# Kernel tuning notes

Hardware: AMD Instinct MI355X
Metric: run time of the kernel (lower is better)

The kernel has to match this reference:

```python
import jax, jax.numpy as jnp
import numpy as np

B, L, C = 32, 8192, 32
P, S = 16, 8
N = (L - P) // S + 1  # 1023 tokens
K = 16
HID = max(16, 2 * K)  # 32
STD_FLOOR = 0.01


def setup_inputs() -> dict:
    key = jax.random.key(0)
    ks = jax.random.split(key, 8)
    return {
        "x": jax.random.normal(ks[0], (B, L, C), jnp.float32),
        "freq_features": jax.random.normal(ks[1], (B * C, N, K), jnp.float32),
        "alpha_w1": jax.random.normal(ks[2], (K, HID), jnp.float32) * 0.1,
        "alpha_b1": jnp.zeros((HID,), jnp.float32),
        "alpha_w2": jax.random.normal(ks[3], (HID, 1), jnp.float32) * 0.1,
        "alpha_b2": jnp.zeros((1,), jnp.float32),
        "beta_w1": jax.random.normal(ks[4], (K, HID), jnp.float32) * 0.1,
        "beta_b1": jnp.zeros((HID,), jnp.float32),
        "beta_w2": jax.random.normal(ks[5], (HID, 1), jnp.float32) * 0.1,
        "beta_b2": jnp.zeros((1,), jnp.float32),
        "affine_scale": jnp.ones((C,), jnp.float32),
        "affine_bias": jnp.zeros((C,), jnp.float32),
        "n_tokens": N,
    }


def _gate_mlp(ff, w1, b1, w2, b2):
    # Linear -> exact GELU (torch default) -> Linear -> sigmoid, squeeze last dim
    h = jax.nn.gelu(ff @ w1 + b1, approximate=False)
    return jax.nn.sigmoid((h @ w2 + b2)[..., 0])


def reference(x, freq_features, alpha_w1, alpha_b1, alpha_w2, alpha_b2,
              beta_w1, beta_b1, beta_w2, beta_b2, affine_scale, affine_bias,
              n_tokens):
    Bx, Lx, Cx = x.shape
    Nn = n_tokens
    # global stats over time dim (biased var)
    mu_g = jnp.mean(x, axis=1, keepdims=True)                     # [B,1,C]
    var_g = jnp.mean((x - mu_g) ** 2, axis=1, keepdims=True)
    std_g = jnp.sqrt(jnp.maximum(var_g, STD_FLOOR * STD_FLOOR))
    # local per-patch stats via strided gather (equivalent to unfold)
    idx = jnp.arange(Nn)[:, None] * S + jnp.arange(P)[None, :]    # [N,P]
    patches = x[:, idx, :]                                        # [B,N,P,C]
    mu_l = jnp.mean(patches, axis=2)                              # [B,N,C]
    var_l = jnp.mean((patches - mu_l[:, :, None, :]) ** 2, axis=2)
    std_l = jnp.sqrt(jnp.maximum(var_l, STD_FLOOR * STD_FLOOR))   # [B,N,C]
    # map each timestep to nearest patch center
    centers = jnp.arange(Nn, dtype=jnp.float32) * S + P / 2.0
    dist = jnp.abs(jnp.arange(Lx, dtype=jnp.float32)[:, None] - centers[None, :])
    tok_per_time = jnp.argmin(dist, axis=1)                       # [L] int
    mu_l_t = mu_l[:, tok_per_time, :]                             # [B,L,C]
    std_l_t = std_l[:, tok_per_time, :]
    # freq-conditioned mixing gate alpha per token, gathered per timestep
    ff = freq_features.reshape(Bx, Cx, Nn, -1)                    # [B,C,N,K]
    alpha_tok = _gate_mlp(ff, alpha_w1, alpha_b1, alpha_w2, alpha_b2)  # [B,C,N]
    beta_tok = _gate_mlp(ff, beta_w1, beta_b1, beta_w2, beta_b2)       # [B,C,N] (ctx only)
    alpha_t = jnp.transpose(alpha_tok[:, :, tok_per_time], (0, 2, 1))  # [B,L,C]
    # normalize and mix
    x_norm_local = jnp.clip((x - mu_l_t) / jnp.maximum(std_l_t, STD_FLOOR), -30.0, 30.0)
    x_norm_global = jnp.clip((x - mu_g) / jnp.maximum(std_g, STD_FLOOR), -30.0, 30.0)
    x_norm = alpha_t * x_norm_local + (1.0 - alpha_t) * x_norm_global
    x_norm = x_norm * affine_scale[None, None, :] + affine_bias[None, None, :]
    return x_norm
```

## Files before the change

kernel.cpp:

```cpp
#include <hip/hip_runtime.h>
#include <math.h>

#define BB   32
#define LL   8192
#define CC   32
#define NTOK 1023
#define KK   16
#define HID  32

typedef short  bf16x8 __attribute__((ext_vector_type(8)));
typedef float  f32x4v __attribute__((ext_vector_type(4)));
typedef unsigned int u32;
typedef unsigned short ushort_t;

__device__ __forceinline__ float4 f4add(float4 a, float4 b) {
    return make_float4(a.x + b.x, a.y + b.y, a.z + b.z, a.w + b.w);
}
__device__ __forceinline__ float4 f4fma(float4 a, float4 b, float4 c) {
    return make_float4(fmaf(a.x, b.x, c.x), fmaf(a.y, b.y, c.y),
                       fmaf(a.z, b.z, c.z), fmaf(a.w, b.w, c.w));
}
__device__ __forceinline__ float4 shflx4(float4 v, int m) {
    return make_float4(__shfl_xor(v.x, m, 64), __shfl_xor(v.y, m, 64),
                       __shfl_xor(v.z, m, 64), __shfl_xor(v.w, m, 64));
}
__device__ __forceinline__ float ex2(float x) {
    return __builtin_amdgcn_exp2f(x);
}
__device__ __forceinline__ u32 pkbf16(float a, float b) {
    u32 r;
    asm("v_cvt_pk_bf16_f32 %0, %1, %2" : "=v"(r) : "v"(a), "v"(b));
    return r;
}

__global__ void __launch_bounds__(256)
kA_fused(const float* __restrict__ x,  const float* __restrict__ ff,
         const float* __restrict__ w1g, const float* __restrict__ b1,
         const float* __restrict__ w2,  const float* __restrict__ b2,
         float* __restrict__ ps, float* __restrict__ pq,
         float* __restrict__ mu_l, float* __restrict__ rstd_l,
         float* __restrict__ alpha_a) {
    __shared__ float4 smem4[592];
    int t   = threadIdx.x;
    int idx = blockIdx.x;
    int r3  = idx % 3, q3 = idx / 3;

    if (r3 == 0) {
        float4* part_s = smem4;
        float4* part_q = part_s + 256;
        float4* halo_s = part_q + 256;
        float4* halo_q = halo_s + 8;
        float4* wred_s = halo_q + 8;
        float4* wred_q = wred_s + 32;

        int b  = q3 >> 5;
        int s  = q3 & 31;
        int c4 = t & 7, rgrp = t >> 3;
        const float4* xb = (const float4*)x + ((size_t)b * LL + s * 256) * 8;

        float4 v[8];
#pragma unroll
        for (int k = 0; k < 8; ++k)
            v[k] = xb[(rgrp * 8 + k) * 8 + c4];
        float4 s4 = make_float4(0.f, 0.f, 0.f, 0.f);
        float4 q4 = make_float4(0.f, 0.f, 0.f, 0.f);
#pragma unroll
        for (int k = 0; k < 8; ++k) {
            s4 = f4add(s4, v[k]);
            q4 = f4fma(v[k], v[k], q4);
        }
        part_s[t] = s4;
        part_q[t] = q4;

        if (t < 64) {
            float4 hs = make_float4(0.f, 0.f, 0.f, 0.f);
            float4 hq = make_float4(0.f, 0.f, 0.f, 0.f);
            if (s < 31) {
                float4 hv = xb[(256 + (t >> 3)) * 8 + c4];
                hs = hv; hq = f4fma(hv, hv, hq);
            }
            hs = f4add(hs, shflx4(hs, 8));  hq = f4add(hq, shflx4(hq, 8));
            hs = f4add(hs, shflx4(hs, 16)); hq = f4add(hq, shflx4(hq, 16));
            hs = f4add(hs, shflx4(hs, 32)); hq = f4add(hq, shflx4(hq, 32));
            if (t < 8) { halo_s[t] = hs; halo_q[t] = hq; }
        }

        float4 gs = s4, gq = q4;
        gs = f4add(gs, shflx4(gs, 8));  gq = f4add(gq, shflx4(gq, 8));
        gs = f4add(gs, shflx4(gs, 16)); gq = f4add(gq, shflx4(gq, 16));
        gs = f4add(gs, shflx4(gs, 32)); gq = f4add(gq, shflx4(gq, 32));
        if ((t & 56) == 0) {
            wred_s[(t >> 6) * 8 + c4] = gs;
            wred_q[(t >> 6) * 8 + c4] = gq;
        }
        __syncthreads();

        int nl = t >> 3;
        int n  = s * 32 + nl;
        if (n < NTOK) {
            float4 a  = (nl < 31) ? part_s[(nl + 1) * 8 + c4] : halo_s[c4];
            float4 bq = (nl < 31) ? part_q[(nl + 1) * 8 + c4] : halo_q[c4];
            float4 ts = f4add(part_s[t], a);
            float4 tq = f4add(part_q[t], bq);
            float4 mu = make_float4(ts.x * 0.0625f, ts.y * 0.0625f,
                                    ts.z * 0.0625f, ts.w * 0.0625f);
            float4 var;
            var.x = fmaxf(fmaf(-mu.x, mu.x, tq.x * 0.0625f), 1e-4f);
            var.y = fmaxf(fmaf(-mu.y, mu.y, tq.y * 0.0625f), 1e-4f);
            var.z = fmaxf(fmaf(-mu.z, mu.z, tq.z * 0.0625f), 1e-4f);
            var.w = fmaxf(fmaf(-mu.w, mu.w, tq.w * 0.0625f), 1e-4f);
            float4 rs = make_float4(1.f / sqrtf(var.x), 1.f / sqrtf(var.y),
                                    1.f / sqrtf(var.z), 1.f / sqrtf(var.w));
            size_t o = (size_t)(b * NTOK + n) * 8 + c4;
            ((float4*)mu_l)[o]   = mu;
            ((float4*)rstd_l)[o] = rs;
        }

        if (t < 8) {
            float4 a = f4add(f4add(wred_s[t], wred_s[8 + t]),
                             f4add(wred_s[16 + t], wred_s[24 + t]));
            float4 c = f4add(f4add(wred_q[t], wred_q[8 + t]),
                             f4add(wred_q[16 + t], wred_q[24 + t]));
            ((float4*)ps)[q3 * 8 + t] = a;
            ((float4*)pq)[q3 * 8 + t] = c;
        }
    } else {
        int a_id = q3 * 2 + (r3 - 1);
        int l  = t & 63, wv = t >> 6;
        bool active = (l < 32);

        int kb = 8 * ((l >> 4) & 1);
        int j0 = l & 15;
        union { u32 w[4]; bf16x8 v; } UA0, UA1;
#pragma unroll
        for (int p = 0; p < 4; ++p) {
            float a0 = w1g[(kb + 2*p)     * HID + j0];
            float a1 = w1g[(kb + 2*p + 1) * HID + j0];
            float a2 = w1g[(kb + 2*p)     * HID + j0 + 16];
            float a3 = w1g[(kb + 2*p + 1) * HID + j0 + 16];
            u32 u0 = pkbf16(a0, a1), u1 = pkbf16(a2, a3);
            UA0.w[p] = active ? u0 : 0u;
            UA1.w[p] = active ? u1 : 0u;
        }
        bf16x8 Alo = UA0.v, Ahi = UA1.v;

        int jg = 4 * (l >> 4);
        f32x4v b1lo = *(const f32x4v*)(b1 + jg);
        f32x4v b1hi = *(const f32x4v*)(b1 + 16 + jg);
        f32x4v w2lo = *(const f32x4v*)(w2 + jg);
        f32x4v w2hi = *(const f32x4v*)(w2 + 16 + jg);
        float b2s = b2[0];

        const float C0 = -2.302211325f;
        const float C1 = -0.102943702f;

        size_t rowbase = ((size_t)a_id * 4 + wv) * 128;
        const float4* fpc = (const float4*)ff + rowbase * 4
                          + (size_t)(l & 15) * 4 + ((l >> 4) & 1) * 2;

        float4 a0 = fpc[0],  a1 = fpc[1];
        float4 p0 = fpc[64], p1 = fpc[65];

        for (int it = 0; it < 8; ++it) {
            float4 f0 = a0, f1 = a1;
            a0 = p0; a1 = p1;
            if (it < 6) { p0 = fpc[128]; p1 = fpc[129]; }
            fpc += 64;

            union { u32 w[4]; bf16x8 v; } B;
            u32 w0 = pkbf16(f0.x, f0.y), w1v = pkbf16(f0.z, f0.w);
            u32 w2v = pkbf16(f1.x, f1.y), w3 = pkbf16(f1.z, f1.w);
            B.w[0] = active ? w0 : 0u;  B.w[1] = active ? w1v : 0u;
            B.w[2] = active ? w2v : 0u; B.w[3] = active ? w3 : 0u;

            f32x4v d0 = __builtin_amdgcn_mfma_f32_16x16x32_bf16(Alo, B.v, b1lo, 0, 0, 0);
            f32x4v d1 = __builtin_amdgcn_mfma_f32_16x16x32_bf16(Ahi, B.v, b1hi, 0, 0, 0);

            float partial = 0.f;
#pragma unroll
            for (int r = 0; r < 4; ++r) {
                float h  = d0[r];
                float a  = fmaf(h * h, C1, C0);
                float g  = h * __builtin_amdgcn_rcpf(1.0f + ex2(a * h));
                partial  = fmaf(g, w2lo[r], partial);
                float h2 = d1[r];
                float a2 = fmaf(h2 * h2, C1, C0);
                float g2 = h2 * __builtin_amdgcn_rcpf(1.0f + ex2(a2 * h2));
                partial  = fmaf(g2, w2hi[r], partial);
            }
            partial += __shfl_xor(partial, 16, 64);
            partial += __shfl_xor(partial, 32, 64);
            float outv = b2s + partial;
            float av = __builtin_amdgcn_rcpf(1.0f + ex2(-1.44269504f * outv));
            if (l < 16) alpha_a[rowbase + l] = av;
            rowbase += 16;
        }
    }
}

__global__ void k3b_transpose(const float* __restrict__ a_bcn,
                              float* __restrict__ a_bnc) {
    __shared__ float tile[32][33];
    int b  = blockIdx.x >> 5;
    int n0 = (blockIdx.x & 31) * 32;
    int tn = threadIdx.x & 31;
    int tc = threadIdx.x >> 5;
#pragma unroll
    for (int i = 0; i < 4; ++i) {
        int c = tc + 8 * i;
        int n = n0 + tn;
        float v = 0.f;
        if (n < NTOK) v = a_bcn[((size_t)(b * CC + c)) * NTOK + n];
        tile[c][tn] = v;
    }
    __syncthreads();
#pragma unroll
    for (int i = 0; i < 4; ++i) {
        int n = n0 + tc + 8 * i;
        if (n < NTOK) a_bnc[((size_t)(b * NTOK + n)) * CC + tn] = tile[tn][tc + 8 * i];
    }
}

__global__ void __launch_bounds__(256)
k4_main(const float4* __restrict__ x4,
        const float* __restrict__ ps, const float* __restrict__ pq,
        const float4* __restrict__ mul4, const float4* __restrict__ rsl4,
        const float4* __restrict__ al4,
        const float4* __restrict__ sc4, const float4* __restrict__ bi4,
        float4* __restrict__ out4) {
    __shared__ float red_s[8][32], red_q[8][32];
    __shared__ float mugs[32], rsgs[32];
    int t  = threadIdx.x;
    int i4 = blockIdx.x * 256 + t;
    int b  = i4 >> 16;

    {
        int c = t & 31, grp = t >> 5;
        float s = 0.f, q = 0.f;
#pragma unroll
        for (int i = 0; i < 4; ++i) {
            int sl = grp * 4 + i;
            s += ps[(b * 32 + sl) * 32 + c];
            q += pq[(b * 32 + sl) * 32 + c];
        }
        red_s[grp][c] = s; red_q[grp][c] = q;
        __syncthreads();
        if (t < 32) {
            float ss = 0.f, qq = 0.f;
#pragma unroll
            for (int g = 0; g < 8; ++g) { ss += red_s[g][t]; qq += red_q[g][t]; }
            float mu  = ss * (1.0f / LL);
            float var = fmaxf(qq * (1.0f / LL) - mu * mu, 1e-4f);
            mugs[t] = mu;
            rsgs[t] = 1.0f / sqrtf(var);
        }
        __syncthreads();
    }

    int c4 = i4 & 7;
    int l  = (i4 >> 3) & (LL - 1);
    int n  = (l >= 5) ? min((l - 5) >> 3, NTOK - 1) : 0;

    float4 xv = x4[i4];
    float4 mg = *(const float4*)(mugs + 4 * c4);
    float4 rg = *(const float4*)(rsgs + 4 * c4);
    int o4 = (b * NTOK + n) * 8 + c4;
    float4 ml = mul4[o4], rl = rsl4[o4], av = al4[o4];
    float4 s  = sc4[c4],  bi = bi4[c4];

    float4 y;
    {
        float xg = fminf(fmaxf((xv.x - mg.x) * rg.x, -30.f), 30.f);
        float xl = fminf(fmaxf((xv.x - ml.x) * rl.x, -30.f), 30.f);
        y.x = fmaf(av.x, xl - xg, xg) * s.x + bi.x;
    }
    {
        float xg = fminf(fmaxf((xv.y - mg.y) * rg.y, -30.f), 30.f);
        float xl = fminf(fmaxf((xv.y - ml.y) * rl.y, -30.f), 30.f);
        y.y = fmaf(av.y, xl - xg, xg) * s.y + bi.y;
    }
    {
        float xg = fminf(fmaxf((xv.z - mg.z) * rg.z, -30.f), 30.f);
        float xl = fminf(fmaxf((xv.z - ml.z) * rl.z, -30.f), 30.f);
        y.z = fmaf(av.z, xl - xg, xg) * s.z + bi.z;
    }
    {
        float xg = fminf(fmaxf((xv.w - mg.w) * rg.w, -30.f), 30.f);
        float xl = fminf(fmaxf((xv.w - ml.w) * rl.w, -30.f), 30.f);
        y.w = fmaf(av.w, xl - xg, xg) * s.w + bi.w;
    }
    out4[i4] = y;
}

extern "C" void kernel_launch(void* const* d_in, const int* in_sizes, int n_in,
                              void* d_out, int out_size, void* d_ws, size_t ws_size,
                              hipStream_t stream) {
    const float* x    = (const float*)d_in[0];
    const float* ff   = (const float*)d_in[1];
    const float* aw1  = (const float*)d_in[2];
    const float* ab1  = (const float*)d_in[3];
    const float* aw2  = (const float*)d_in[4];
    const float* ab2  = (const float*)d_in[5];
    const float* scal = (const float*)d_in[10];
    const float* bias = (const float*)d_in[11];
    float* out = (float*)d_out;

    float* wsf     = (float*)d_ws;
    float* ps      = wsf;
    float* pq      = wsf + 32768;
    float* mu_l    = wsf + 65536;
    float* rstd_l  = mu_l    + 1047552;
    float* alpha_a = rstd_l  + 1047552;
    float* alpha_t = alpha_a + 1047552;

    kA_fused<<<3070, 256, 0, stream>>>(x, ff, aw1, ab1, aw2, ab2,
                                       ps, pq, mu_l, rstd_l, alpha_a);
    k3b_transpose<<<BB * 32, 256, 0, stream>>>(alpha_a, alpha_t);
    k4_main<<<8192, 256, 0, stream>>>((const float4*)x, ps, pq,
                                      (const float4*)mu_l, (const float4*)rstd_l,
                                      (const float4*)alpha_t,
                                      (const float4*)scal, (const float4*)bias,
                                      (float4*)out);
}
```

Before: 47.61 us.

## Fuse alpha gate transpose into MLP kernel via shared-memory tile

The separate transpose kernel that converted the alpha gate from [B,C,N] to [B,N,C] is removed. Each MLP workgroup now handles 16 tokens across all 32 channels of one batch, keeps the 32x16 results in shared memory and writes them out already transposed. This removes one launch and a full write-then-read round trip of the alpha buffer. In exchange the freq-feature loads become strided by channel, token indices at the tail are clamped, and the grid grows slightly to 3072 blocks.

```diff
diff --git a/kernel.cpp b/kernel.cpp
--- a/kernel.cpp
+++ b/kernel.cpp
@@ -39,7 +39,7 @@
          const float* __restrict__ w2,  const float* __restrict__ b2,
          float* __restrict__ ps, float* __restrict__ pq,
          float* __restrict__ mu_l, float* __restrict__ rstd_l,
-         float* __restrict__ alpha_a) {
+         float* __restrict__ alpha_t) {
     __shared__ float4 smem4[592];
     int t   = threadIdx.x;
     int idx = blockIdx.x;
@@ -125,7 +125,10 @@
             ((float4*)pq)[q3 * 8 + t] = c;
         }
     } else {
+        float* als = (float*)smem4;
         int a_id = q3 * 2 + (r3 - 1);
+        int b    = a_id >> 6;
+        int n0   = (a_id & 63) * 16;
         int l  = t & 63, wv = t >> 6;
         bool active = (l < 32);
 
@@ -154,18 +157,20 @@
         const float C0 = -2.302211325f;
         const float C1 = -0.102943702f;
 
-        size_t rowbase = ((size_t)a_id * 4 + wv) * 128;
-        const float4* fpc = (const float4*)ff + rowbase * 4
-                          + (size_t)(l & 15) * 4 + ((l >> 4) & 1) * 2;
-
-        float4 a0 = fpc[0],  a1 = fpc[1];
-        float4 p0 = fpc[64], p1 = fpc[65];
+        int nlane = min(n0 + (l & 15), NTOK - 1);
+        size_t cbase = (size_t)(b * 32 + 8 * wv) * NTOK;
+        const float4* fpc = (const float4*)ff + (cbase + nlane) * 4
+                          + ((l >> 4) & 1) * 2;
+        const int STRD = NTOK * 4;
+
+        float4 a0 = fpc[0],     a1 = fpc[1];
+        float4 p0 = fpc[STRD],  p1 = fpc[STRD + 1];
 
         for (int it = 0; it < 8; ++it) {
             float4 f0 = a0, f1 = a1;
             a0 = p0; a1 = p1;
-            if (it < 6) { p0 = fpc[128]; p1 = fpc[129]; }
-            fpc += 64;
+            if (it < 6) { p0 = fpc[2 * STRD]; p1 = fpc[2 * STRD + 1]; }
+            fpc += STRD;
 
             union { u32 w[4]; bf16x8 v; } B;
             u32 w0 = pkbf16(f0.x, f0.y), w1v = pkbf16(f0.z, f0.w);
@@ -192,32 +197,18 @@
             partial += __shfl_xor(partial, 32, 64);
             float outv = b2s + partial;
             float av = __builtin_amdgcn_rcpf(1.0f + ex2(-1.44269504f * outv));
-            if (l < 16) alpha_a[rowbase + l] = av;
-            rowbase += 16;
-        }
-    }
-}
-
-__global__ void k3b_transpose(const float* __restrict__ a_bcn,
-                              float* __restrict__ a_bnc) {
-    __shared__ float tile[32][33];
-    int b  = blockIdx.x >> 5;
-    int n0 = (blockIdx.x & 31) * 32;
-    int tn = threadIdx.x & 31;
-    int tc = threadIdx.x >> 5;
-#pragma unroll
-    for (int i = 0; i < 4; ++i) {
-        int c = tc + 8 * i;
-        int n = n0 + tn;
-        float v = 0.f;
-        if (n < NTOK) v = a_bcn[((size_t)(b * CC + c)) * NTOK + n];
-        tile[c][tn] = v;
-    }
-    __syncthreads();
-#pragma unroll
-    for (int i = 0; i < 4; ++i) {
-        int n = n0 + tc + 8 * i;
-        if (n < NTOK) a_bnc[((size_t)(b * NTOK + n)) * CC + tn] = tile[tn][tc + 8 * i];
+            if (l < 16) als[(8 * wv + it) * 17 + l] = av;
+        }
+        __syncthreads();
+
+        int flat = t * 2;
+        int nn = flat >> 5, cc = flat & 31;
+        if (n0 + nn < NTOK) {
+            float2 o;
+            o.x = als[cc * 17 + nn];
+            o.y = als[(cc + 1) * 17 + nn];
+            *(float2*)(alpha_t + ((size_t)(b * NTOK + n0 + nn)) * CC + cc) = o;
+        }
     }
 }
 
@@ -310,12 +301,10 @@
     float* pq      = wsf + 32768;
     float* mu_l    = wsf + 65536;
     float* rstd_l  = mu_l    + 1047552;
-    float* alpha_a = rstd_l  + 1047552;
-    float* alpha_t = alpha_a + 1047552;
-
-    kA_fused<<<3070, 256, 0, stream>>>(x, ff, aw1, ab1, aw2, ab2,
-                                       ps, pq, mu_l, rstd_l, alpha_a);
-    k3b_transpose<<<BB * 32, 256, 0, stream>>>(alpha_a, alpha_t);
+    float* alpha_t = rstd_l  + 1047552;
+
+    kA_fused<<<3072, 256, 0, stream>>>(x, ff, aw1, ab1, aw2, ab2,
+                                       ps, pq, mu_l, rstd_l, alpha_t);
     k4_main<<<8192, 256, 0, stream>>>((const float4*)x, ps, pq,
                                       (const float4*)mu_l, (const float4*)rstd_l,
                                       (const float4*)alpha_t,
```

New measurement: 42.51 us. 1.12x faster.
